# Performance work log

Measured on AMD Instinct MI355X. Metric: run time of the kernel, lower is better.

Reference implementation:

```python
import jax, jax.numpy as jnp
import numpy as np


def setup_inputs() -> dict:
    key = jax.random.key(0)
    k1, k2 = jax.random.split(key)
    out = jax.random.uniform(k1, (32, 128, 128, 9, 5), dtype=jnp.float32)
    target = jax.random.uniform(k2, (32, 128, 128, 3, 6), dtype=jnp.float32)
    return {"out": out, "target": target}


def _loss(out, target):
    # out: [B, GX, GY, A, 5], target: [B, GX, GY, Q, 6]
    B, GX, GY, Q, _ = target.shape
    A = out.shape[3]
    # the original loop breaks after qub == 0, so only the first gt per cell is used
    st = target[:, :, :, 0, :]            # [B, GX, GY, 6]
    pos = st[..., 5] > 0.8                # [B, GX, GY] positive-cell mask

    dtype = out.dtype
    # grid-cell centers zxdwx / zxdwy
    zx = (jnp.arange(GX, dtype=dtype) / GX + 1.0 / (2 * GX))[None, :, None, None]
    zy = (jnp.arange(GY, dtype=dtype) / GY + 1.0 / (2 * GY))[None, None, :, None]

    # gt box (center format) -> corners; broadcast over anchor dim
    acx = st[..., 0][..., None]
    acy = st[..., 1][..., None]
    aw = st[..., 2][..., None]
    ah = st[..., 3][..., None]
    ax1, ay1, ax2, ay2 = acx - aw / 2, acy - ah / 2, acx + aw / 2, acy + ah / 2

    # predicted box: offsets decoded relative to grid cell
    bcx = out[..., 0] - 0.5 + zx
    bcy = out[..., 1] - 0.5 + zy
    bw = out[..., 2] - 0.5 + 1.0 / GX
    bh = out[..., 3] - 0.5 + 1.0 / GY
    bx1, by1, bx2, by2 = bcx - bw / 2, bcy - bh / 2, bcx + bw / 2, bcy + bh / 2

    # IoU (intersection zeroed when either overlap extent <= 0)
    iw = jnp.minimum(ax2, bx2) - jnp.maximum(ax1, bx1)
    ih = jnp.minimum(ay2, by2) - jnp.maximum(ay1, by1)
    cross = jnp.where((iw > 0) & (ih > 0), iw * ih, 0.0)
    area_a = (ax2 - ax1) * (ay2 - ay1)
    area_b = (bx2 - bx1) * (by2 - by1)
    union = area_a + area_b - cross
    iou = cross / (union + 1e-6)

    # DIoU term: center distance over bound-box diagonal
    d = jnp.sqrt(((bx1 + bx2) / 2 - (ax1 + ax2) / 2) ** 2
                 + ((by1 + by2) / 2 - (ay1 + ay2) / 2) ** 2)
    cx1 = jnp.minimum(ax1, bx1)
    cy1 = jnp.minimum(ay1, by1)
    cx2 = jnp.maximum(ax2, bx2)
    cy2 = jnp.maximum(ay2, by2)
    c = jnp.sqrt((cx2 - cx1) ** 2 + (cy2 - cy1) ** 2)
    diou = iou - d ** 2 / c ** 2

    # CIoU aspect-ratio term
    v = (4.0 / np.pi ** 2) * (jnp.arctan((ax2 - ax1) / (ay2 - ay1))
                              - jnp.arctan((bx2 - bx1) / (by2 - by1))) ** 2
    alpha = v / (1 - iou + v)
    los = 1 - (diou - alpha * v)      # [B, GX, GY, A]

    obj = out[..., 4]
    posA = pos[..., None]             # broadcast mask over anchors

    jsq = (jnp.sum(pos) * A).astype(dtype)
    qit = (jnp.sum(~pos) * A).astype(dtype)
    allloss = jnp.sum(jnp.where(posA, los + (1 - obj), 0.0))
    jbb = jnp.sum(jnp.where(posA, iou, 0.0))
    huhuh = jnp.sum(jnp.where(posA, 1 - obj, 0.0))
    zsd = jnp.sum(jnp.where(posA, (1 - obj) ** 2, obj ** 2))

    return (allloss / jsq + zsd / (jsq + qit), jbb / jsq, huhuh / jsq)


def reference(out, target):
    return _loss(out, target)
```

## Files before the change

### kernel.cpp

```cpp
#include <hip/hip_runtime.h>
#include <math.h>

constexpr int kGX     = 128;
constexpr int kGY     = 128;
constexpr int kA      = 9;
constexpr int kNCells = 32 * kGX * kGY;
constexpr int kN      = kNCells * kA;

constexpr int kCellsPerTile = 16;
constexpr int kTiles  = kNCells / kCellsPerTile;
constexpr int kBlocks = kTiles / 4;
static_assert(kBlocks * 4 == kTiles, "exact cover");

constexpr int kOutF4  = kCellsPerTile * 45 / 4;
constexpr int kTgtF4  = kCellsPerTile * 18 / 4;
constexpr int kTileF4 = kOutF4 + kTgtF4;

__device__ inline void gload_lds16(const void* gptr, void* lptr) {
    __builtin_amdgcn_global_load_lds(
        (const __attribute__((address_space(1))) unsigned int*)gptr,
        (__attribute__((address_space(3))) unsigned int*)lptr, 16, 0, 0);
}

__device__ inline float frcp(float x) { return __builtin_amdgcn_rcpf(x); }

__device__ inline float fast_atan(float r) {
    const float x = fabsf(r);
    const bool inv = x > 1.f;
    const float t = inv ? frcp(x) : x;
    const float t2 = t * t;
    float p = fmaf(t2, 0.0208351f, -0.0851330f);
    p = fmaf(t2, p, 0.1801410f);
    p = fmaf(t2, p, -0.3302995f);
    p = fmaf(t2, p, 0.9998660f);
    p = t * p;
    float res = inv ? (1.5707963f - p) : p;
    return r < 0.f ? -res : res;
}

__global__ __launch_bounds__(256, 8)
void loss_main(const float* __restrict__ outp, const float* __restrict__ tgt,
               double* __restrict__ acc, int mode) {
    __shared__ float4 s_tile[4 * kTileF4];
    __shared__ float smem[4][5];

    const int lane = threadIdx.x & 63;
    const int wv   = threadIdx.x >> 6;
    float4* sw = s_tile + wv * kTileF4;
    const float* swf = (const float*)sw;
    const int tile = blockIdx.x * 4 + wv;

    {
        const float4* g = (const float4*)outp + (size_t)tile * kOutF4;
        gload_lds16(&g[lane], &sw[lane]);
        gload_lds16(&g[64 + lane], &sw[64 + lane]);
        if (lane < kOutF4 - 128) gload_lds16(&g[128 + lane], &sw[128 + lane]);
        const float4* h = (const float4*)tgt + (size_t)tile * kTgtF4;
        gload_lds16(&h[lane], &sw[kOutF4 + lane]);
        if (lane < kTgtF4 - 64) gload_lds16(&h[64 + lane], &sw[kOutF4 + 64 + lane]);
    }
    __builtin_amdgcn_s_waitcnt(0);

    const int c = lane >> 2;
    const int p = lane & 3;
    const int cell = tile * kCellsPerTile + c;
    const int gy = cell & (kGY - 1);
    const int gx = (cell >> 7) & (kGX - 1);

    const float* st = swf + 4 * kOutF4 + c * 18;
    const float acx = st[0], acy = st[1], aw = st[2], ah = st[3], conf = st[5];
    const bool pos = conf > 0.8f;

    const float zx = (float)gx * (1.f / kGX) + 0.5f / kGX;
    const float zy = (float)gy * (1.f / kGY) + 0.5f / kGY;
    const float ax1 = acx - 0.5f * aw, ax2 = acx + 0.5f * aw;
    const float ay1 = acy - 0.5f * ah, ay2 = acy + 0.5f * ah;
    const float area_a = aw * ah;
    const float atan_a = fast_atan(aw * frcp(ah));

    const float* ob = swf + c * 45 + p * 5;

    float t_all = 0.f, t_jbb = 0.f, t_huh = 0.f, t_zsd = 0.f;
    float t_jsq = pos ? (p == 0 ? 3.f : 2.f) : 0.f;

    #pragma unroll
    for (int k = 0; k < 3; ++k) {
        const int a = p + 4 * k;
        const bool act = (a < kA);
        const int off = act ? k * 20 : 0;
        const float o0 = ob[off + 0], o1 = ob[off + 1], o2 = ob[off + 2];
        const float o3 = ob[off + 3], obj = ob[off + 4];

        const float bcx = o0 - 0.5f + zx;
        const float bcy = o1 - 0.5f + zy;
        const float bw  = o2 - 0.5f + (1.f / kGX);
        const float bh  = o3 - 0.5f + (1.f / kGY);
        const float bx1 = bcx - 0.5f * bw, bx2 = bcx + 0.5f * bw;
        const float by1 = bcy - 0.5f * bh, by2 = bcy + 0.5f * bh;

        const float iw = fminf(ax2, bx2) - fmaxf(ax1, bx1);
        const float ih = fminf(ay2, by2) - fmaxf(ay1, by1);
        const float cross = (iw > 0.f && ih > 0.f) ? iw * ih : 0.f;
        const float uni = area_a + bw * bh - cross;
        const float iou = cross * frcp(uni + 1e-6f);

        const float dx = bcx - acx, dy = bcy - acy;
        const float d2 = dx * dx + dy * dy;
        const float cw  = fmaxf(ax2, bx2) - fminf(ax1, bx1);
        const float chh = fmaxf(ay2, by2) - fminf(ay1, by1);
        const float c2 = cw * cw + chh * chh;
        const float diou = iou - d2 * frcp(c2);

        const float dat = atan_a - fast_atan(bw * frcp(bh));
        const float v = 0.4052847345693511f * dat * dat;
        const float alpha = v * frcp(1.f - iou + v);
        const float los = 1.f - (diou - alpha * v);
        const float om = 1.f - obj;

        const bool pp = pos && act;
        t_all += pp ? (los + om) : 0.f;
        t_jbb += pp ? iou : 0.f;
        t_huh += pp ? om : 0.f;
        t_zsd += pp ? om * om : (act ? obj * obj : 0.f);
    }

    float vals[5] = {t_jsq, t_all, t_jbb, t_huh, t_zsd};
    #pragma unroll
    for (int i = 0; i < 5; ++i) {
        float x = vals[i];
        #pragma unroll
        for (int off = 32; off > 0; off >>= 1) x += __shfl_down(x, off, 64);
        vals[i] = x;
    }
    if (lane == 0) {
        #pragma unroll
        for (int i = 0; i < 5; ++i) smem[wv][i] = vals[i];
    }
    __syncthreads();
    if (threadIdx.x < 5) {
        const double sv = (double)smem[0][threadIdx.x] + (double)smem[1][threadIdx.x] +
                          (double)smem[2][threadIdx.x] + (double)smem[3][threadIdx.x];
        if (mode) acc[(size_t)blockIdx.x * 5 + threadIdx.x] = sv;
        else atomicAdd(&acc[threadIdx.x], sv);
    }
}

__global__ __launch_bounds__(256)
void loss_final(const double* __restrict__ acc, float* __restrict__ res, int n_part) {
    if (n_part > 0) {
        double v[5] = {0, 0, 0, 0, 0};
        for (int j = threadIdx.x; j < n_part; j += 256) {
            #pragma unroll
            for (int i = 0; i < 5; ++i) v[i] += acc[(size_t)j * 5 + i];
        }
        #pragma unroll
        for (int i = 0; i < 5; ++i) {
            double x = v[i];
            #pragma unroll
            for (int off = 32; off > 0; off >>= 1) x += __shfl_down(x, off, 64);
            v[i] = x;
        }
        __shared__ double sm[4][5];
        const int lane = threadIdx.x & 63, wv = threadIdx.x >> 6;
        if (lane == 0) {
            #pragma unroll
            for (int i = 0; i < 5; ++i) sm[wv][i] = v[i];
        }
        __syncthreads();
        if (threadIdx.x == 0) {
            #pragma unroll
            for (int i = 0; i < 5; ++i) v[i] = sm[0][i] + sm[1][i] + sm[2][i] + sm[3][i];
            const double jsq = v[0], total = (double)kN;
            res[0] = (float)(v[1] / jsq + v[4] / total);
            res[1] = (float)(v[2] / jsq);
            res[2] = (float)(v[3] / jsq);
        }
    } else if (threadIdx.x == 0) {
        const double jsq = acc[0], total = (double)kN;
        res[0] = (float)(acc[1] / jsq + acc[4] / total);
        res[1] = (float)(acc[2] / jsq);
        res[2] = (float)(acc[3] / jsq);
    }
}

extern "C" void kernel_launch(void* const* d_in, const int* in_sizes, int n_in,
                              void* d_out, int out_size, void* d_ws, size_t ws_size,
                              hipStream_t stream) {
    const float* outp = (const float*)d_in[0];
    const float* tgt  = (const float*)d_in[1];
    float* res = (float*)d_out;
    double* acc = (double*)d_ws;

    const bool partials = ws_size >= (size_t)kBlocks * 5 * sizeof(double);
    if (!partials) hipMemsetAsync(acc, 0, 5 * sizeof(double), stream);
    loss_main<<<kBlocks, 256, 0, stream>>>(outp, tgt, acc, partials ? 1 : 0);
    loss_final<<<1, 256, 0, stream>>>(acc, res, partials ? kBlocks : 0);
}
```

Before: 175.9 us.

## Loop each wave over eight tiles with double-buffered async LDS prefetch

Each wave now processes eight consecutive tiles instead of one. It stages the next tile into a second LDS buffer with global_load_lds while computing the current one, and waits only on the older loads through an explicit vmcnt. This cuts the grid size and the number of per-block partial sums, and is meant to hide global-load latency behind the IoU math. In exchange, fewer waves are launched, LDS per block doubles and the occupancy hint is dropped, so less memory parallelism may come from wave count.

```diff
diff --git a/kernel.cpp b/kernel.cpp
--- a/kernel.cpp
+++ b/kernel.cpp
@@ -9,12 +9,17 @@
 
 constexpr int kCellsPerTile = 16;
 constexpr int kTiles  = kNCells / kCellsPerTile;
-constexpr int kBlocks = kTiles / 4;
-static_assert(kBlocks * 4 == kTiles, "exact cover");
+constexpr int kT      = 8;
+constexpr int kWaves  = kTiles / kT;
+constexpr int kBlocks = kWaves / 4;
+static_assert(kBlocks * 4 * kT == kTiles, "exact cover");
 
 constexpr int kOutF4  = kCellsPerTile * 45 / 4;
 constexpr int kTgtF4  = kCellsPerTile * 18 / 4;
 constexpr int kTileF4 = kOutF4 + kTgtF4;
+
+#define WAITCNT_VM5  0x0F75
+#define WAITCNT_VM0  0x0F70
 
 __device__ inline void gload_lds16(const void* gptr, void* lptr) {
     __builtin_amdgcn_global_load_lds(
@@ -38,90 +43,104 @@
     return r < 0.f ? -res : res;
 }
 
-__global__ __launch_bounds__(256, 8)
+__global__ __launch_bounds__(256)
 void loss_main(const float* __restrict__ outp, const float* __restrict__ tgt,
                double* __restrict__ acc, int mode) {
-    __shared__ float4 s_tile[4 * kTileF4];
+    __shared__ float4 s_tile[4 * 2 * kTileF4];
     __shared__ float smem[4][5];
 
     const int lane = threadIdx.x & 63;
     const int wv   = threadIdx.x >> 6;
-    float4* sw = s_tile + wv * kTileF4;
-    const float* swf = (const float*)sw;
-    const int tile = blockIdx.x * 4 + wv;
-
-    {
-        const float4* g = (const float4*)outp + (size_t)tile * kOutF4;
-        gload_lds16(&g[lane], &sw[lane]);
-        gload_lds16(&g[64 + lane], &sw[64 + lane]);
-        if (lane < kOutF4 - 128) gload_lds16(&g[128 + lane], &sw[128 + lane]);
-        const float4* h = (const float4*)tgt + (size_t)tile * kTgtF4;
-        gload_lds16(&h[lane], &sw[kOutF4 + lane]);
-        if (lane < kTgtF4 - 64) gload_lds16(&h[64 + lane], &sw[kOutF4 + 64 + lane]);
-    }
-    __builtin_amdgcn_s_waitcnt(0);
+    float4* sb = s_tile + wv * (2 * kTileF4);
+    const int tile0 = (blockIdx.x * 4 + wv) * kT;
 
     const int c = lane >> 2;
     const int p = lane & 3;
-    const int cell = tile * kCellsPerTile + c;
-    const int gy = cell & (kGY - 1);
-    const int gx = (cell >> 7) & (kGX - 1);
-
-    const float* st = swf + 4 * kOutF4 + c * 18;
-    const float acx = st[0], acy = st[1], aw = st[2], ah = st[3], conf = st[5];
-    const bool pos = conf > 0.8f;
-
-    const float zx = (float)gx * (1.f / kGX) + 0.5f / kGX;
-    const float zy = (float)gy * (1.f / kGY) + 0.5f / kGY;
-    const float ax1 = acx - 0.5f * aw, ax2 = acx + 0.5f * aw;
-    const float ay1 = acy - 0.5f * ah, ay2 = acy + 0.5f * ah;
-    const float area_a = aw * ah;
-    const float atan_a = fast_atan(aw * frcp(ah));
-
-    const float* ob = swf + c * 45 + p * 5;
-
-    float t_all = 0.f, t_jbb = 0.f, t_huh = 0.f, t_zsd = 0.f;
-    float t_jsq = pos ? (p == 0 ? 3.f : 2.f) : 0.f;
-
-    #pragma unroll
-    for (int k = 0; k < 3; ++k) {
-        const int a = p + 4 * k;
-        const bool act = (a < kA);
-        const int off = act ? k * 20 : 0;
-        const float o0 = ob[off + 0], o1 = ob[off + 1], o2 = ob[off + 2];
-        const float o3 = ob[off + 3], obj = ob[off + 4];
-
-        const float bcx = o0 - 0.5f + zx;
-        const float bcy = o1 - 0.5f + zy;
-        const float bw  = o2 - 0.5f + (1.f / kGX);
-        const float bh  = o3 - 0.5f + (1.f / kGY);
-        const float bx1 = bcx - 0.5f * bw, bx2 = bcx + 0.5f * bw;
-        const float by1 = bcy - 0.5f * bh, by2 = bcy + 0.5f * bh;
-
-        const float iw = fminf(ax2, bx2) - fmaxf(ax1, bx1);
-        const float ih = fminf(ay2, by2) - fmaxf(ay1, by1);
-        const float cross = (iw > 0.f && ih > 0.f) ? iw * ih : 0.f;
-        const float uni = area_a + bw * bh - cross;
-        const float iou = cross * frcp(uni + 1e-6f);
-
-        const float dx = bcx - acx, dy = bcy - acy;
-        const float d2 = dx * dx + dy * dy;
-        const float cw  = fmaxf(ax2, bx2) - fminf(ax1, bx1);
-        const float chh = fmaxf(ay2, by2) - fminf(ay1, by1);
-        const float c2 = cw * cw + chh * chh;
-        const float diou = iou - d2 * frcp(c2);
-
-        const float dat = atan_a - fast_atan(bw * frcp(bh));
-        const float v = 0.4052847345693511f * dat * dat;
-        const float alpha = v * frcp(1.f - iou + v);
-        const float los = 1.f - (diou - alpha * v);
-        const float om = 1.f - obj;
-
-        const bool pp = pos && act;
-        t_all += pp ? (los + om) : 0.f;
-        t_jbb += pp ? iou : 0.f;
-        t_huh += pp ? om : 0.f;
-        t_zsd += pp ? om * om : (act ? obj * obj : 0.f);
+
+    auto stage = [&](int t, int buf) {
+        const float4* g = (const float4*)outp + (size_t)(tile0 + t) * kOutF4;
+        float4* d = sb + buf * kTileF4;
+        gload_lds16(&g[lane], &d[lane]);
+        gload_lds16(&g[64 + lane], &d[64 + lane]);
+        if (lane < kOutF4 - 128) gload_lds16(&g[128 + lane], &d[128 + lane]);
+        const float4* h = (const float4*)tgt + (size_t)(tile0 + t) * kTgtF4;
+        gload_lds16(&h[lane], &d[kOutF4 + lane]);
+        if (lane < kTgtF4 - 64) gload_lds16(&h[64 + lane], &d[kOutF4 + 64 + lane]);
+    };
+
+    float t_jsq = 0.f, t_all = 0.f, t_jbb = 0.f, t_huh = 0.f, t_zsd = 0.f;
+
+    stage(0, 0);
+
+    for (int t = 0; t < kT; ++t) {
+        if (t + 1 < kT) {
+            stage(t + 1, (t + 1) & 1);
+            __builtin_amdgcn_s_waitcnt(WAITCNT_VM5);
+        } else {
+            __builtin_amdgcn_s_waitcnt(WAITCNT_VM0);
+        }
+
+        const float* swf = (const float*)(sb + (t & 1) * kTileF4);
+        const int tile = tile0 + t;
+        const int cell = tile * kCellsPerTile + c;
+        const int gy = cell & (kGY - 1);
+        const int gx = (cell >> 7) & (kGX - 1);
+
+        const float* st = swf + 4 * kOutF4 + c * 18;
+        const float acx = st[0], acy = st[1], aw = st[2], ah = st[3], conf = st[5];
+        const bool pos = conf > 0.8f;
+
+        const float zx = (float)gx * (1.f / kGX) + 0.5f / kGX;
+        const float zy = (float)gy * (1.f / kGY) + 0.5f / kGY;
+        const float ax1 = acx - 0.5f * aw, ax2 = acx + 0.5f * aw;
+        const float ay1 = acy - 0.5f * ah, ay2 = acy + 0.5f * ah;
+        const float area_a = aw * ah;
+        const float atan_a = fast_atan(aw * frcp(ah));
+
+        const float* ob = swf + c * 45 + p * 5;
+
+        t_jsq += pos ? (p == 0 ? 3.f : 2.f) : 0.f;
+
+        #pragma unroll
+        for (int k = 0; k < 3; ++k) {
+            const int a = p + 4 * k;
+            const bool act = (a < kA);
+            const int off = act ? k * 20 : 0;
+            const float o0 = ob[off + 0], o1 = ob[off + 1], o2 = ob[off + 2];
+            const float o3 = ob[off + 3], obj = ob[off + 4];
+
+            const float bcx = o0 - 0.5f + zx;
+            const float bcy = o1 - 0.5f + zy;
+            const float bw  = o2 - 0.5f + (1.f / kGX);
+            const float bh  = o3 - 0.5f + (1.f / kGY);
+            const float bx1 = bcx - 0.5f * bw, bx2 = bcx + 0.5f * bw;
+            const float by1 = bcy - 0.5f * bh, by2 = bcy + 0.5f * bh;
+
+            const float iw = fminf(ax2, bx2) - fmaxf(ax1, bx1);
+            const float ih = fminf(ay2, by2) - fmaxf(ay1, by1);
+            const float cross = (iw > 0.f && ih > 0.f) ? iw * ih : 0.f;
+            const float uni = area_a + bw * bh - cross;
+            const float iou = cross * frcp(uni + 1e-6f);
+
+            const float dx = bcx - acx, dy = bcy - acy;
+            const float d2 = dx * dx + dy * dy;
+            const float cw  = fmaxf(ax2, bx2) - fminf(ax1, bx1);
+            const float chh = fmaxf(ay2, by2) - fminf(ay1, by1);
+            const float c2 = cw * cw + chh * chh;
+            const float diou = iou - d2 * frcp(c2);
+
+            const float dat = atan_a - fast_atan(bw * frcp(bh));
+            const float v = 0.4052847345693511f * dat * dat;
+            const float alpha = v * frcp(1.f - iou + v);
+            const float los = 1.f - (diou - alpha * v);
+            const float om = 1.f - obj;
+
+            const bool pp = pos && act;
+            t_all += pp ? (los + om) : 0.f;
+            t_jbb += pp ? iou : 0.f;
+            t_huh += pp ? om : 0.f;
+            t_zsd += pp ? om * om : (act ? obj * obj : 0.f);
+        }
     }
 
     float vals[5] = {t_jsq, t_all, t_jbb, t_huh, t_zsd};
```

Measured after the change: 174.0 us. No clear change (-1.1%).

## Map each thread to four consecutive anchors with direct float4 global loads

Applied to the files above, without the earlier changes.

Replaces the per-wave LDS staging of 16-cell tiles with a flat mapping: each thread reads five float4s (four anchors) straight from global memory and gathers the target record for up to two cells. This removes LDS traffic, the async-load wait and the idle lanes of the old 4-lanes-per-cell scheme (one in four k-iterations was inactive). In exchange, target reads are redundant across threads and uncoalesced, and each thread does extra selects and a second atan per record. Grid size grows to one thread per four anchors.

```diff
diff --git a/kernel.cpp b/kernel.cpp
--- a/kernel.cpp
+++ b/kernel.cpp
@@ -7,20 +7,9 @@
 constexpr int kNCells = 32 * kGX * kGY;
 constexpr int kN      = kNCells * kA;
 
-constexpr int kCellsPerTile = 16;
-constexpr int kTiles  = kNCells / kCellsPerTile;
-constexpr int kBlocks = kTiles / 4;
-static_assert(kBlocks * 4 == kTiles, "exact cover");
-
-constexpr int kOutF4  = kCellsPerTile * 45 / 4;
-constexpr int kTgtF4  = kCellsPerTile * 18 / 4;
-constexpr int kTileF4 = kOutF4 + kTgtF4;
-
-__device__ inline void gload_lds16(const void* gptr, void* lptr) {
-    __builtin_amdgcn_global_load_lds(
-        (const __attribute__((address_space(1))) unsigned int*)gptr,
-        (__attribute__((address_space(3))) unsigned int*)lptr, 16, 0, 0);
-}
+constexpr int kGroups = kN / 4;
+constexpr int kBlocks = kGroups / 256;
+static_assert(kBlocks * 256 * 4 == kN, "exact cover");
 
 __device__ inline float frcp(float x) { return __builtin_amdgcn_rcpf(x); }
 
@@ -38,58 +27,65 @@
     return r < 0.f ? -res : res;
 }
 
-__global__ __launch_bounds__(256, 8)
+struct Rec {
+    float ax1, ax2, ay1, ay2, acx, acy, area, atg, zx, zy, posf;
+};
+
+__device__ inline Rec make_rec(const float* __restrict__ tgt, int cell) {
+    const float2* t2p = (const float2*)(tgt + (size_t)cell * 18);
+    const float2 a01 = t2p[0];
+    const float2 a23 = t2p[1];
+    const float conf = ((const float*)t2p)[5];
+    Rec r;
+    r.acx = a01.x; r.acy = a01.y;
+    r.ax1 = a01.x - 0.5f * a23.x; r.ax2 = a01.x + 0.5f * a23.x;
+    r.ay1 = a01.y - 0.5f * a23.y; r.ay2 = a01.y + 0.5f * a23.y;
+    r.area = a23.x * a23.y;
+    r.atg  = fast_atan(a23.x * frcp(a23.y));
+    const int gy = cell & (kGY - 1);
+    const int gx = (cell >> 7) & (kGX - 1);
+    r.zx = (float)gx * (1.f / kGX) + 0.5f / kGX;
+    r.zy = (float)gy * (1.f / kGY) + 0.5f / kGY;
+    r.posf = (conf > 0.8f) ? 1.f : 0.f;
+    return r;
+}
+
+__global__ __launch_bounds__(256)
 void loss_main(const float* __restrict__ outp, const float* __restrict__ tgt,
                double* __restrict__ acc, int mode) {
-    __shared__ float4 s_tile[4 * kTileF4];
-    __shared__ float smem[4][5];
+    const int gid = blockIdx.x * 256 + threadIdx.x;
+    const int a0  = gid * 4;
 
-    const int lane = threadIdx.x & 63;
-    const int wv   = threadIdx.x >> 6;
-    float4* sw = s_tile + wv * kTileF4;
-    const float* swf = (const float*)sw;
-    const int tile = blockIdx.x * 4 + wv;
+    const float4* o4 = (const float4*)outp + (size_t)gid * 5;
+    const float4 q0 = o4[0], q1 = o4[1], q2 = o4[2], q3 = o4[3], q4 = o4[4];
 
-    {
-        const float4* g = (const float4*)outp + (size_t)tile * kOutF4;
-        gload_lds16(&g[lane], &sw[lane]);
-        gload_lds16(&g[64 + lane], &sw[64 + lane]);
-        if (lane < kOutF4 - 128) gload_lds16(&g[128 + lane], &sw[128 + lane]);
-        const float4* h = (const float4*)tgt + (size_t)tile * kTgtF4;
-        gload_lds16(&h[lane], &sw[kOutF4 + lane]);
-        if (lane < kTgtF4 - 64) gload_lds16(&h[64 + lane], &sw[kOutF4 + 64 + lane]);
-    }
-    __builtin_amdgcn_s_waitcnt(0);
+    const int cell0 = (int)(__umulhi((unsigned)a0, 0x38E38E39u) >> 1);
+    const int r0    = a0 - cell0 * 9;
+    const int cell1 = min(cell0 + 1, kNCells - 1);
 
-    const int c = lane >> 2;
-    const int p = lane & 3;
-    const int cell = tile * kCellsPerTile + c;
-    const int gy = cell & (kGY - 1);
-    const int gx = (cell >> 7) & (kGX - 1);
+    const Rec RA = make_rec(tgt, cell0);
+    const Rec RB = make_rec(tgt, cell1);
 
-    const float* st = swf + 4 * kOutF4 + c * 18;
-    const float acx = st[0], acy = st[1], aw = st[2], ah = st[3], conf = st[5];
-    const bool pos = conf > 0.8f;
+    const float o[20] = {q0.x, q0.y, q0.z, q0.w, q1.x, q1.y, q1.z, q1.w,
+                         q2.x, q2.y, q2.z, q2.w, q3.x, q3.y, q3.z, q3.w,
+                         q4.x, q4.y, q4.z, q4.w};
 
-    const float zx = (float)gx * (1.f / kGX) + 0.5f / kGX;
-    const float zy = (float)gy * (1.f / kGY) + 0.5f / kGY;
-    const float ax1 = acx - 0.5f * aw, ax2 = acx + 0.5f * aw;
-    const float ay1 = acy - 0.5f * ah, ay2 = acy + 0.5f * ah;
-    const float area_a = aw * ah;
-    const float atan_a = fast_atan(aw * frcp(ah));
-
-    const float* ob = swf + c * 45 + p * 5;
-
-    float t_all = 0.f, t_jbb = 0.f, t_huh = 0.f, t_zsd = 0.f;
-    float t_jsq = pos ? (p == 0 ? 3.f : 2.f) : 0.f;
+    float t_jsq = 0.f, t_all = 0.f, t_jbb = 0.f, t_huh = 0.f, t_zsd = 0.f;
 
     #pragma unroll
-    for (int k = 0; k < 3; ++k) {
-        const int a = p + 4 * k;
-        const bool act = (a < kA);
-        const int off = act ? k * 20 : 0;
-        const float o0 = ob[off + 0], o1 = ob[off + 1], o2 = ob[off + 2];
-        const float o3 = ob[off + 3], obj = ob[off + 4];
+    for (int j = 0; j < 4; ++j) {
+        const bool cross = (r0 + j) >= 9;
+        const float ax1 = cross ? RB.ax1 : RA.ax1, ax2 = cross ? RB.ax2 : RA.ax2;
+        const float ay1 = cross ? RB.ay1 : RA.ay1, ay2 = cross ? RB.ay2 : RA.ay2;
+        const float acx = cross ? RB.acx : RA.acx, acy = cross ? RB.acy : RA.acy;
+        const float area_a = cross ? RB.area : RA.area;
+        const float atan_a = cross ? RB.atg : RA.atg;
+        const float zx = cross ? RB.zx : RA.zx, zy = cross ? RB.zy : RA.zy;
+        const float posf = cross ? RB.posf : RA.posf;
+        const bool pos = posf > 0.5f;
+
+        const float o0 = o[j * 5 + 0], o1 = o[j * 5 + 1], o2 = o[j * 5 + 2];
+        const float o3 = o[j * 5 + 3], obj = o[j * 5 + 4];
 
         const float bcx = o0 - 0.5f + zx;
         const float bcy = o1 - 0.5f + zy;
@@ -100,9 +96,9 @@
 
         const float iw = fminf(ax2, bx2) - fmaxf(ax1, bx1);
         const float ih = fminf(ay2, by2) - fmaxf(ay1, by1);
-        const float cross = (iw > 0.f && ih > 0.f) ? iw * ih : 0.f;
-        const float uni = area_a + bw * bh - cross;
-        const float iou = cross * frcp(uni + 1e-6f);
+        const float cross_a = (iw > 0.f && ih > 0.f) ? iw * ih : 0.f;
+        const float uni = area_a + bw * bh - cross_a;
+        const float iou = cross_a * frcp(uni + 1e-6f);
 
         const float dx = bcx - acx, dy = bcy - acy;
         const float d2 = dx * dx + dy * dy;
@@ -117,13 +113,15 @@
         const float los = 1.f - (diou - alpha * v);
         const float om = 1.f - obj;
 
-        const bool pp = pos && act;
-        t_all += pp ? (los + om) : 0.f;
-        t_jbb += pp ? iou : 0.f;
-        t_huh += pp ? om : 0.f;
-        t_zsd += pp ? om * om : (act ? obj * obj : 0.f);
+        t_jsq += posf;
+        t_all += pos ? (los + om) : 0.f;
+        t_jbb += pos ? iou : 0.f;
+        t_huh += pos ? om : 0.f;
+        t_zsd += pos ? om * om : obj * obj;
     }
 
+    const int lane = threadIdx.x & 63;
+    const int wv   = threadIdx.x >> 6;
     float vals[5] = {t_jsq, t_all, t_jbb, t_huh, t_zsd};
     #pragma unroll
     for (int i = 0; i < 5; ++i) {
@@ -132,6 +130,7 @@
         for (int off = 32; off > 0; off >>= 1) x += __shfl_down(x, off, 64);
         vals[i] = x;
     }
+    __shared__ float smem[4][5];
     if (lane == 0) {
         #pragma unroll
         for (int i = 0; i < 5; ++i) smem[wv][i] = vals[i];
```

Result: faster. 170.4 us (-3.1%).
